# Kernel tuning notes

Hardware: AMD Instinct MI355X
Metric: run time of the kernel (lower is better)

## Reference

```python
import jax, jax.numpy as jnp
import numpy as np

N_NODES = 50000
N_EDGES = 800000
IN_F = 128
HID = 128
N_REL = 8


def setup_inputs() -> dict:
    key = jax.random.key(0)
    ks = jax.random.split(key, 12)
    s = 0.05
    return {
        "in_feat": jax.random.normal(ks[0], (N_NODES, IN_F), dtype=jnp.float32),
        "W1": jax.random.normal(ks[1], (N_REL, IN_F, HID), dtype=jnp.float32) * s,
        "W1_self": jax.random.normal(ks[2], (IN_F, HID), dtype=jnp.float32) * s,
        "b1": jnp.zeros((HID,), dtype=jnp.float32),
        "W2": jax.random.normal(ks[3], (N_REL, HID, HID), dtype=jnp.float32) * s,
        "W2_self": jax.random.normal(ks[4], (HID, HID), dtype=jnp.float32) * s,
        "b2": jnp.zeros((HID,), dtype=jnp.float32),
        "fc_w": jax.random.normal(ks[5], (HID, 1), dtype=jnp.float32) * s,
        "fc_b": jnp.zeros((1,), dtype=jnp.float32),
        "src": jax.random.randint(ks[6], (N_EDGES,), 0, N_NODES),
        "dst": jax.random.randint(ks[7], (N_EDGES,), 0, N_NODES),
        "etypes": jax.random.randint(ks[8], (N_EDGES,), 0, N_REL),
    }


def _rel_graph_conv(h, W, W_self, b, src, dst, etypes, n_nodes):
    # Transform node features once per relation: [R, N, H]
    xr = jnp.einsum('nd,rdh->rnh', h, W)
    # Per-edge message: gather relation-specific transformed source features [E, H]
    msgs = xr[etypes, src]
    # Scatter-sum aggregation to destination nodes [N, H]
    agg = jax.ops.segment_sum(msgs, dst, num_segments=n_nodes)
    # Self-loop + bias + ReLU (DGL RelGraphConv defaults)
    return jax.nn.relu(agg + h @ W_self + b)


def reference(in_feat, W1, W1_self, b1, W2, W2_self, b2, fc_w, fc_b, src, dst, etypes):
    n = in_feat.shape[0]
    h = _rel_graph_conv(in_feat, W1, W1_self, b1, src, dst, etypes, n)
    # dropout layers are identity in eval mode
    h = _rel_graph_conv(h, W2, W2_self, b2, src, dst, etypes, n)
    pooled = jnp.mean(h, axis=0, keepdims=True)  # AvgPooling over one graph -> [1, H]
    logits = pooled @ fc_w + fc_b                # [1, 1]
    return jax.nn.sigmoid(logits)
```

## Files before the change

### kernel.cpp

```cpp
#include <hip/hip_runtime.h>

#define NNODES 50000
#define NEDGES 800000
#define F 128
#define NREL 8
#define NOUT 1152
#define NBKT 98
#define BSH 9
#define SEG 16384
#define NTILES 391
#define GEMM_BLOCKS (8 * 9 * 49)
#define CSR_BLOCKS 196

typedef short bf16x8 __attribute__((ext_vector_type(8)));
typedef float f32x4 __attribute__((ext_vector_type(4)));
typedef float f32x2 __attribute__((ext_vector_type(2)));

__device__ __forceinline__ unsigned f2bf(float f) {
  unsigned u = __float_as_uint(f);
  u += 0x7fffu + ((u >> 16) & 1u);
  return u >> 16;
}
__device__ __forceinline__ float bf2f(unsigned v) {
  return __uint_as_float(v << 16);
}

typedef __attribute__((address_space(3))) void lds_void;
typedef const __attribute__((address_space(1))) void glb_void;
__device__ __forceinline__ void gll16(const void* g, void* l) {
  __builtin_amdgcn_global_load_lds(
      (glb_void*)(unsigned long long)g,
      (lds_void*)(unsigned)(unsigned long long)l, 16, 0, 0);
}

#define PREP_ZERO  33
#define PREP_CVT   12500
#define PREP_W     576
__global__ __launch_bounds__(256)
void k_prep(const float* __restrict__ in_feat, ushort* __restrict__ feat0,
            const float* __restrict__ W1, const float* __restrict__ W1s,
            ushort* __restrict__ Wt1,
            const float* __restrict__ W2, const float* __restrict__ W2s,
            ushort* __restrict__ Wt2,
            float* __restrict__ pooled_p, int* __restrict__ bcur) {
  const int b = blockIdx.x, t = threadIdx.x;
  if (b < 32) {
    pooled_p[b * 256 + t] = 0.f;
  } else if (b < PREP_ZERO) {
    if (t <= NBKT) bcur[t] = 0;
  } else if (b < PREP_ZERO + PREP_CVT) {
    int i = (b - PREP_ZERO) * 256 + t;
    float2 v = ((const float2*)in_feat)[i];
    ((unsigned*)feat0)[i] = f2bf(v.x) | (f2bf(v.y) << 16);
  } else {
    int w2 = (b >= PREP_ZERO + PREP_CVT + PREP_W);
    int idx = (b - PREP_ZERO - PREP_CVT - (w2 ? PREP_W : 0)) * 256 + t;
    int n = idx >> 7, k = idx & 127;
    int r = n >> 7, c = n & 127;
    const float* Wr = w2 ? W2 : W1;
    const float* Ws = w2 ? W2s : W1s;
    float v = (r < NREL) ? Wr[((size_t)r * F + k) * F + c] : Ws[(size_t)k * F + c];
    (w2 ? Wt2 : Wt1)[idx] = (ushort)f2bf(v);
  }
}

__global__ __launch_bounds__(256)
void k_fsort(const int* __restrict__ ebuf, const int* __restrict__ bcur,
             int* __restrict__ rowptr, int* __restrict__ edata) {
  __shared__ int cnt[512];
  __shared__ int pos[512];
  __shared__ int ws2[256];
  __shared__ int bc_s;
  const int b = blockIdx.x, t = threadIdx.x;
  int myc = (t < NBKT) ? bcur[t] : 0;
  ws2[t] = (t < b) ? myc : 0;
  if (t == b) bc_s = myc;
  __syncthreads();
  for (int off = 1; off < 256; off <<= 1) {
    int x = (t >= off) ? ws2[t - off] : 0;
    __syncthreads();
    ws2[t] += x;
    __syncthreads();
  }
  const int beg = ws2[255];
  const int cntb = bc_s;
  const int sbeg = b * SEG;

  cnt[t] = 0; cnt[t + 256] = 0;
  __syncthreads();
  for (int e = t; e < cntb; e += 256)
    atomicAdd(&cnt[((unsigned)ebuf[sbeg + e]) >> 19], 1);
  __syncthreads();
  int a = cnt[2 * t], b2 = cnt[2 * t + 1];
  ws2[t] = a + b2;
  __syncthreads();
  for (int off = 1; off < 256; off <<= 1) {
    int x = (t >= off) ? ws2[t - off] : 0;
    __syncthreads();
    ws2[t] += x;
    __syncthreads();
  }
  int ep = ws2[t] - (a + b2);
  pos[2 * t] = ep;
  pos[2 * t + 1] = ep + a;
  __syncthreads();
  int node0 = b << BSH;
#pragma unroll
  for (int i = t; i < 512; i += 256) {
    int node = node0 + i;
    if (node < NNODES) rowptr[node] = beg + pos[i];
  }
  if (b == NBKT - 1 && t == 0) rowptr[NNODES] = NEDGES;
  __syncthreads();
  for (int e = t; e < cntb; e += 256) {
    int rec = ebuf[sbeg + e];
    int c = ((unsigned)rec) >> 19;
    int lrank = atomicAdd(&pos[c], 1);
    int srcv = (rec >> 3) & 0xFFFF;
    int etv = rec & 7;
    edata[beg + lrank] = srcv * NOUT + etv * F;
  }
}

__global__ __launch_bounds__(512, 4)
void gemm_xrs(const ushort* __restrict__ A, const ushort* __restrict__ Wt,
              unsigned char* __restrict__ xrs, int doCsr,
              const int* __restrict__ src, const int* __restrict__ dst,
              const int* __restrict__ et, int* __restrict__ bcur,
              int* __restrict__ ebuf) {
  __shared__ uint4 As[2048];
  __shared__ uint4 Bs[2048];
  __shared__ int lhist[NBKT];
  __shared__ int lbase[NBKT];
  const int tid = threadIdx.x;

  if (doCsr && blockIdx.x < CSR_BLOCKS) {
    if (tid < NBKT) lhist[tid] = 0;
    __syncthreads();
    int e0 = blockIdx.x * 4096;
    int rec[8], cc[8], lr[8];
#pragma unroll
    for (int i = 0; i < 8; ++i) {
      int e = e0 + tid + i * 512;
      if (e < NEDGES) {
        int d = dst[e];
        cc[i] = d >> BSH;
        rec[i] = ((d & 511) << 19) | (src[e] << 3) | et[e];
        lr[i] = atomicAdd(&lhist[cc[i]], 1);
      } else {
        cc[i] = -1;
      }
    }
    __syncthreads();
    if (tid < NBKT && lhist[tid] > 0) lbase[tid] = atomicAdd(&bcur[tid], lhist[tid]);
    __syncthreads();
#pragma unroll
    for (int i = 0; i < 8; ++i)
      if (cc[i] >= 0) ebuf[cc[i] * SEG + lbase[cc[i]] + lr[i]] = rec[i];
    return;
  }

  const int id = blockIdx.x - (doCsr ? CSR_BLOCKS : 0);
  const int x = id & 7, j = id >> 3;
  const int tile = (j / 9) * 8 + x;
  const int cb = j % 9;
  if (tile >= NTILES) return;
  const int row0 = tile * 128;

  const int lane = tid & 63;
  const int w = tid >> 6;
  const int i16 = lane & 15, q = lane >> 4;
  const int mbase = (w & 3) * 32, nbase = (w >> 2) * 64;

#pragma unroll
  for (int i = 0; i < 4; ++i) {
    int L = tid + i * 512;
    int r = L >> 4, c4s = L & 15;
    int c4 = c4s ^ (r & 15);
    int agr = row0 + r; if (agr >= NNODES) agr = NNODES - 1;
    gll16((const void*)(A + (size_t)agr * F + c4 * 8), (void*)&As[L]);
    gll16((const void*)(Wt + ((size_t)cb * 128 + r) * F + c4 * 8), (void*)&Bs[L]);
  }
  __syncthreads();

  f32x4 acc[2][4];
#pragma unroll
  for (int a = 0; a < 2; ++a)
#pragma unroll
    for (int b = 0; b < 4; ++b) acc[a][b] = (f32x4)0.f;

#pragma unroll
  for (int c = 0; c < 4; ++c) {
    bf16x8 af[2], bfr[4];
#pragma unroll
    for (int mi = 0; mi < 2; ++mi) {
      int r = mbase + mi * 16 + i16;
      af[mi] = *(const bf16x8*)&As[r * 16 + ((c * 4 + q) ^ (r & 15))];
    }
#pragma unroll
    for (int ni = 0; ni < 4; ++ni) {
      int r = nbase + ni * 16 + i16;
      bfr[ni] = *(const bf16x8*)&Bs[r * 16 + ((c * 4 + q) ^ (r & 15))];
    }
#pragma unroll
    for (int mi = 0; mi < 2; ++mi)
#pragma unroll
      for (int ni = 0; ni < 4; ++ni)
        acc[mi][ni] = __builtin_amdgcn_mfma_f32_16x16x32_bf16(
            bfr[ni], af[mi], acc[mi][ni], 0, 0, 0);
  }

  unsigned pkv[2][4];
#pragma unroll
  for (int mi = 0; mi < 2; ++mi)
#pragma unroll
    for (int ni = 0; ni < 4; ++ni) {
      f32x4 v = acc[mi][ni];
      unsigned pk = 0;
      pk = __builtin_amdgcn_cvt_pk_fp8_f32(v[0], v[1], pk, false);
      pk = __builtin_amdgcn_cvt_pk_fp8_f32(v[2], v[3], pk, true);
      pkv[mi][ni] = pk;
    }

  __syncthreads();
  unsigned* sbuf = (unsigned*)As;
  {
    const int dbase = (nbase >> 2) + q;
#pragma unroll
    for (int mi = 0; mi < 2; ++mi) {
      int nl = mbase + mi * 16 + i16;
      int sw = (nl & 7) << 2;
      int vb_ = nl * 32;
#pragma unroll
      for (int ni = 0; ni < 4; ++ni)
        sbuf[vb_ + ((dbase + ni * 4) ^ sw)] = pkv[mi][ni];
    }
  }
  __syncthreads();

#pragma unroll
  for (int k = 0; k < 2; ++k) {
    int nl = k * 64 + (tid >> 3);
    int ch = tid & 7;
    int d0 = (ch * 4) ^ ((nl & 7) << 2);
    uint4 v = *(const uint4*)&sbuf[nl * 32 + d0];
    int row = row0 + nl;
    if (row < NNODES)
      *(uint4*)(xrs + (size_t)row * NOUT + cb * 128 + ch * 16) = v;
  }
}

__global__ __launch_bounds__(256)
void k_aggregate(const unsigned char* __restrict__ xrs,
                 const int* __restrict__ rowptr, const int* __restrict__ edata,
                 const float* __restrict__ bias, ushort* __restrict__ hout,
                 float* __restrict__ pooled_p) {
  __shared__ float red[4][128];
  const int wv = threadIdx.x >> 6;
  const int node = blockIdx.x * 4 + wv;
  const int lane = threadIdx.x & 63;
  const int half = lane >> 5, sl = lane & 31;
  const int beg = rowptr[node], end = rowptr[node + 1];

  float a0 = 0.f, a1 = 0.f, a2 = 0.f, a3 = 0.f;
  if (half == 0) {
    unsigned sv = *(const unsigned*)(xrs + (size_t)node * NOUT + NREL * F + sl * 4);
    f32x2 lo = __builtin_amdgcn_cvt_pk_f32_fp8(sv, false);
    f32x2 hi = __builtin_amdgcn_cvt_pk_f32_fp8(sv, true);
    a0 += lo[0]; a1 += lo[1]; a2 += hi[0]; a3 += hi[1];
  }

  for (int base = beg; base < end; base += 64) {
    int cnt = end - base; if (cnt > 64) cnt = 64;
    int my = (base + lane < end) ? edata[base + lane] : 0;
    int pairs = cnt >> 1;
    int p = 0;
    for (; p + 8 <= pairs; p += 8) {
      unsigned v[8];
#pragma unroll
      for (int k = 0; k < 8; ++k) {
        int off = __shfl(my, 2 * (p + k) + half, 64);
        v[k] = *(const unsigned*)(xrs + (size_t)off + sl * 4);
      }
#pragma unroll
      for (int k = 0; k < 8; ++k) {
        f32x2 lo = __builtin_amdgcn_cvt_pk_f32_fp8(v[k], false);
        f32x2 hi = __builtin_amdgcn_cvt_pk_f32_fp8(v[k], true);
        a0 += lo[0]; a1 += lo[1]; a2 += hi[0]; a3 += hi[1];
      }
    }
    for (; p < pairs; ++p) {
      int off = __shfl(my, 2 * p + half, 64);
      unsigned vv = *(const unsigned*)(xrs + (size_t)off + sl * 4);
      f32x2 lo = __builtin_amdgcn_cvt_pk_f32_fp8(vv, false);
      f32x2 hi = __builtin_amdgcn_cvt_pk_f32_fp8(vv, true);
      a0 += lo[0]; a1 += lo[1]; a2 += hi[0]; a3 += hi[1];
    }
    if (cnt & 1) {
      int off = __shfl(my, cnt - 1, 64);
      if (half == 0) {
        unsigned vv = *(const unsigned*)(xrs + (size_t)off + sl * 4);
        f32x2 lo = __builtin_amdgcn_cvt_pk_f32_fp8(vv, false);
        f32x2 hi = __builtin_amdgcn_cvt_pk_f32_fp8(vv, true);
        a0 += lo[0]; a1 += lo[1]; a2 += hi[0]; a3 += hi[1];
      }
    }
  }

  a0 += __shfl_xor(a0, 32, 64);
  a1 += __shfl_xor(a1, 32, 64);
  a2 += __shfl_xor(a2, 32, 64);
  a3 += __shfl_xor(a3, 32, 64);

  float4 bb = ((const float4*)bias)[sl];
  a0 = fmaxf(a0 + bb.x, 0.f);
  a1 = fmaxf(a1 + bb.y, 0.f);
  a2 = fmaxf(a2 + bb.z, 0.f);
  a3 = fmaxf(a3 + bb.w, 0.f);

  if (hout) {
    if (half == 0) {
      uint2 pk;
      pk.x = f2bf(a0) | (f2bf(a1) << 16);
      pk.y = f2bf(a2) | (f2bf(a3) << 16);
      ((uint2*)(hout + (size_t)node * F))[sl] = pk;
    }
  } else {
    if (half == 0) {
      red[wv][sl * 4 + 0] = a0;
      red[wv][sl * 4 + 1] = a1;
      red[wv][sl * 4 + 2] = a2;
      red[wv][sl * 4 + 3] = a3;
    }
    __syncthreads();
    if (threadIdx.x < 128) {
      float s = red[0][threadIdx.x] + red[1][threadIdx.x] +
                red[2][threadIdx.x] + red[3][threadIdx.x];
      atomicAdd(&pooled_p[(blockIdx.x & 63) * 128 + threadIdx.x], s);
    }
  }
}

__global__ __launch_bounds__(128)
void k_final(const float* __restrict__ pooled_p, const float* __restrict__ fcw,
             const float* __restrict__ fcb, float* __restrict__ out) {
  __shared__ float s[128];
  int t = threadIdx.x;
  float acc = 0.f;
#pragma unroll 8
  for (int k = 0; k < 64; ++k) acc += pooled_p[k * 128 + t];
  s[t] = acc * (1.0f / (float)NNODES) * fcw[t];
  __syncthreads();
  if (t == 0) {
    float v = 0.f;
    for (int i = 0; i < 128; ++i) v += s[i];
    v += fcb[0];
    out[0] = 1.f / (1.f + expf(-v));
  }
}

extern "C" void kernel_launch(void* const* d_in, const int* in_sizes, int n_in,
                              void* d_out, int out_size, void* d_ws, size_t ws_size,
                              hipStream_t stream) {
  const float* in_feat = (const float*)d_in[0];
  const float* W1      = (const float*)d_in[1];
  const float* W1s     = (const float*)d_in[2];
  const float* b1      = (const float*)d_in[3];
  const float* W2      = (const float*)d_in[4];
  const float* W2s     = (const float*)d_in[5];
  const float* b2      = (const float*)d_in[6];
  const float* fcw     = (const float*)d_in[7];
  const float* fcb     = (const float*)d_in[8];
  const int*   src     = (const int*)d_in[9];
  const int*   dst     = (const int*)d_in[10];
  const int*   et      = (const int*)d_in[11];
  float* out = (float*)d_out;

  unsigned char* xrs = (unsigned char*)d_ws;
  ushort* feat0 = (ushort*)(xrs + (size_t)NNODES * NOUT);
  ushort* h1    = feat0 + (size_t)NNODES * F;
  ushort* Wt1   = h1 + (size_t)NNODES * F;
  ushort* Wt2   = Wt1 + (size_t)NOUT * F;
  float* pooled_p = (float*)(Wt2 + (size_t)NOUT * F);
  int*   bcur   = (int*)(pooled_p + 64 * 128);
  int*   rowptr = bcur + NBKT + 1;
  int*   ebuf   = rowptr + NNODES + 2;
  int*   edata  = ebuf + NBKT * SEG;

  k_prep<<<PREP_ZERO + PREP_CVT + 2 * PREP_W, 256, 0, stream>>>(
      in_feat, feat0, W1, W1s, Wt1, W2, W2s, Wt2, pooled_p, bcur);

  const int aggBlocks = NNODES / 4;

  gemm_xrs<<<CSR_BLOCKS + GEMM_BLOCKS, 512, 0, stream>>>(
      feat0, Wt1, xrs, 1, src, dst, et, bcur, ebuf);
  k_fsort<<<NBKT, 256, 0, stream>>>(ebuf, bcur, rowptr, edata);
  k_aggregate<<<aggBlocks, 256, 0, stream>>>(xrs, rowptr, edata, b1, h1, nullptr);
  gemm_xrs<<<GEMM_BLOCKS, 512, 0, stream>>>(
      h1, Wt2, xrs, 0, src, dst, et, bcur, ebuf);
  k_aggregate<<<aggBlocks, 256, 0, stream>>>(xrs, rowptr, edata, b2, nullptr, pooled_p);

  k_final<<<1, 128, 0, stream>>>(pooled_p, fcw, fcb, out);
}
```

Baseline: 231.8 us.

## Switch GEMM operands and intermediate features from bf16 to fp8

Input features, weights and the layer-1 hidden output are now stored as fp8 (e4m3) instead of bf16, and the GEMM uses the fp8 MFMA with halved LDS tiles and an adjusted swizzle. This halves the bytes of the A/B operands loaded per tile and shrinks the prep conversion and h1 write traffic, and the halved LDS allows a higher occupancy launch bound. It costs accuracy, since inputs and weights are quantized to 8-bit floats before the matmul, which may push the result past tolerance.

```diff
diff --git a/kernel.cpp b/kernel.cpp
--- a/kernel.cpp
+++ b/kernel.cpp
@@ -12,7 +12,6 @@
 #define GEMM_BLOCKS (8 * 9 * 49)
 #define CSR_BLOCKS 196
 
-typedef short bf16x8 __attribute__((ext_vector_type(8)));
 typedef float f32x4 __attribute__((ext_vector_type(4)));
 typedef float f32x2 __attribute__((ext_vector_type(2)));
 
@@ -20,9 +19,6 @@
   unsigned u = __float_as_uint(f);
   u += 0x7fffu + ((u >> 16) & 1u);
   return u >> 16;
-}
-__device__ __forceinline__ float bf2f(unsigned v) {
-  return __uint_as_float(v << 16);
 }
 
 typedef __attribute__((address_space(3))) void lds_void;
@@ -34,14 +30,14 @@
 }
 
 #define PREP_ZERO  33
-#define PREP_CVT   12500
-#define PREP_W     576
+#define PREP_CVT   6250
+#define PREP_W     144
 __global__ __launch_bounds__(256)
-void k_prep(const float* __restrict__ in_feat, ushort* __restrict__ feat0,
+void k_prep(const float* __restrict__ in_feat, unsigned* __restrict__ feat0,
             const float* __restrict__ W1, const float* __restrict__ W1s,
-            ushort* __restrict__ Wt1,
+            unsigned* __restrict__ Wt1,
             const float* __restrict__ W2, const float* __restrict__ W2s,
-            ushort* __restrict__ Wt2,
+            unsigned* __restrict__ Wt2,
             float* __restrict__ pooled_p, int* __restrict__ bcur) {
   const int b = blockIdx.x, t = threadIdx.x;
   if (b < 32) {
@@ -50,17 +46,34 @@
     if (t <= NBKT) bcur[t] = 0;
   } else if (b < PREP_ZERO + PREP_CVT) {
     int i = (b - PREP_ZERO) * 256 + t;
-    float2 v = ((const float2*)in_feat)[i];
-    ((unsigned*)feat0)[i] = f2bf(v.x) | (f2bf(v.y) << 16);
+    float4 v = ((const float4*)in_feat)[i];
+    unsigned pk = 0;
+    pk = __builtin_amdgcn_cvt_pk_fp8_f32(v.x, v.y, pk, false);
+    pk = __builtin_amdgcn_cvt_pk_fp8_f32(v.z, v.w, pk, true);
+    feat0[i] = pk;
   } else {
     int w2 = (b >= PREP_ZERO + PREP_CVT + PREP_W);
     int idx = (b - PREP_ZERO - PREP_CVT - (w2 ? PREP_W : 0)) * 256 + t;
-    int n = idx >> 7, k = idx & 127;
+    int n = idx >> 5, k0 = (idx & 31) * 4;
     int r = n >> 7, c = n & 127;
     const float* Wr = w2 ? W2 : W1;
     const float* Ws = w2 ? W2s : W1s;
-    float v = (r < NREL) ? Wr[((size_t)r * F + k) * F + c] : Ws[(size_t)k * F + c];
-    (w2 ? Wt2 : Wt1)[idx] = (ushort)f2bf(v);
+    float v0, v1, v2, v3;
+    if (r < NREL) {
+      v0 = Wr[((size_t)(r * F + k0 + 0)) * F + c];
+      v1 = Wr[((size_t)(r * F + k0 + 1)) * F + c];
+      v2 = Wr[((size_t)(r * F + k0 + 2)) * F + c];
+      v3 = Wr[((size_t)(r * F + k0 + 3)) * F + c];
+    } else {
+      v0 = Ws[(size_t)(k0 + 0) * F + c];
+      v1 = Ws[(size_t)(k0 + 1) * F + c];
+      v2 = Ws[(size_t)(k0 + 2) * F + c];
+      v3 = Ws[(size_t)(k0 + 3) * F + c];
+    }
+    unsigned pk = 0;
+    pk = __builtin_amdgcn_cvt_pk_fp8_f32(v0, v1, pk, false);
+    pk = __builtin_amdgcn_cvt_pk_fp8_f32(v2, v3, pk, true);
+    (w2 ? Wt2 : Wt1)[idx] = pk;
   }
 }
 
@@ -122,14 +135,15 @@
   }
 }
 
-__global__ __launch_bounds__(512, 4)
-void gemm_xrs(const ushort* __restrict__ A, const ushort* __restrict__ Wt,
+__global__ __launch_bounds__(512, 8)
+void gemm_xrs(const unsigned char* __restrict__ A,
+              const unsigned char* __restrict__ Wt,
               unsigned char* __restrict__ xrs, int doCsr,
               const int* __restrict__ src, const int* __restrict__ dst,
               const int* __restrict__ et, int* __restrict__ bcur,
               int* __restrict__ ebuf) {
-  __shared__ uint4 As[2048];
-  __shared__ uint4 Bs[2048];
+  __shared__ uint4 As[1024];
+  __shared__ uint4 Bs[1024];
   __shared__ int lhist[NBKT];
   __shared__ int lbase[NBKT];
   const int tid = threadIdx.x;
@@ -173,13 +187,13 @@
   const int mbase = (w & 3) * 32, nbase = (w >> 2) * 64;
 
 #pragma unroll
-  for (int i = 0; i < 4; ++i) {
+  for (int i = 0; i < 2; ++i) {
     int L = tid + i * 512;
-    int r = L >> 4, c4s = L & 15;
-    int c4 = c4s ^ (r & 15);
+    int r = L >> 3, c8s = L & 7;
+    int c8 = c8s ^ (r & 7);
     int agr = row0 + r; if (agr >= NNODES) agr = NNODES - 1;
-    gll16((const void*)(A + (size_t)agr * F + c4 * 8), (void*)&As[L]);
-    gll16((const void*)(Wt + ((size_t)cb * 128 + r) * F + c4 * 8), (void*)&Bs[L]);
+    gll16((const void*)(A + (size_t)agr * F + c8 * 16), (void*)&As[L]);
+    gll16((const void*)(Wt + ((size_t)cb * 128 + r) * F + c8 * 16), (void*)&Bs[L]);
   }
   __syncthreads();
 
@@ -189,24 +203,28 @@
 #pragma unroll
     for (int b = 0; b < 4; ++b) acc[a][b] = (f32x4)0.f;
 
+  const char* Ab = (const char*)As;
+  const char* Bb = (const char*)Bs;
 #pragma unroll
   for (int c = 0; c < 4; ++c) {
-    bf16x8 af[2], bfr[4];
+    const int ch = c * 2 + (q >> 1);
+    const int h8 = (q & 1) << 3;
+    long af[2], bfr[4];
 #pragma unroll
     for (int mi = 0; mi < 2; ++mi) {
       int r = mbase + mi * 16 + i16;
-      af[mi] = *(const bf16x8*)&As[r * 16 + ((c * 4 + q) ^ (r & 15))];
+      af[mi] = *(const long*)(Ab + r * 128 + ((ch ^ (r & 7)) << 4) + h8);
     }
 #pragma unroll
     for (int ni = 0; ni < 4; ++ni) {
       int r = nbase + ni * 16 + i16;
-      bfr[ni] = *(const bf16x8*)&Bs[r * 16 + ((c * 4 + q) ^ (r & 15))];
+      bfr[ni] = *(const long*)(Bb + r * 128 + ((ch ^ (r & 7)) << 4) + h8);
     }
 #pragma unroll
     for (int mi = 0; mi < 2; ++mi)
 #pragma unroll
       for (int ni = 0; ni < 4; ++ni)
-        acc[mi][ni] = __builtin_amdgcn_mfma_f32_16x16x32_bf16(
+        acc[mi][ni] = __builtin_amdgcn_mfma_f32_16x16x32_fp8_fp8(
             bfr[ni], af[mi], acc[mi][ni], 0, 0, 0);
   }
 
@@ -253,7 +271,7 @@
 __global__ __launch_bounds__(256)
 void k_aggregate(const unsigned char* __restrict__ xrs,
                  const int* __restrict__ rowptr, const int* __restrict__ edata,
-                 const float* __restrict__ bias, ushort* __restrict__ hout,
+                 const float* __restrict__ bias, unsigned char* __restrict__ hout,
                  float* __restrict__ pooled_p) {
   __shared__ float red[4][128];
   const int wv = threadIdx.x >> 6;
@@ -320,10 +338,10 @@
 
   if (hout) {
     if (half == 0) {
-      uint2 pk;
-      pk.x = f2bf(a0) | (f2bf(a1) << 16);
-      pk.y = f2bf(a2) | (f2bf(a3) << 16);
-      ((uint2*)(hout + (size_t)node * F))[sl] = pk;
+      unsigned pk = 0;
+      pk = __builtin_amdgcn_cvt_pk_fp8_f32(a0, a1, pk, false);
+      pk = __builtin_amdgcn_cvt_pk_fp8_f32(a2, a3, pk, true);
+      ((unsigned*)(hout + (size_t)node * F))[sl] = pk;
     }
   } else {
     if (half == 0) {
@@ -377,10 +395,10 @@
   float* out = (float*)d_out;
 
   unsigned char* xrs = (unsigned char*)d_ws;
-  ushort* feat0 = (ushort*)(xrs + (size_t)NNODES * NOUT);
-  ushort* h1    = feat0 + (size_t)NNODES * F;
-  ushort* Wt1   = h1 + (size_t)NNODES * F;
-  ushort* Wt2   = Wt1 + (size_t)NOUT * F;
+  unsigned char* feat0 = xrs + (size_t)NNODES * NOUT;
+  unsigned char* h1  = feat0 + (size_t)NNODES * F;
+  unsigned char* Wt1 = h1 + (size_t)NNODES * F;
+  unsigned char* Wt2 = Wt1 + (size_t)NOUT * F;
   float* pooled_p = (float*)(Wt2 + (size_t)NOUT * F);
   int*   bcur   = (int*)(pooled_p + 64 * 128);
   int*   rowptr = bcur + NBKT + 1;
@@ -388,7 +406,8 @@
   int*   edata  = ebuf + NBKT * SEG;
 
   k_prep<<<PREP_ZERO + PREP_CVT + 2 * PREP_W, 256, 0, stream>>>(
-      in_feat, feat0, W1, W1s, Wt1, W2, W2s, Wt2, pooled_p, bcur);
+      in_feat, (unsigned*)feat0, W1, W1s, (unsigned*)Wt1,
+      W2, W2s, (unsigned*)Wt2, pooled_p, bcur);
 
   const int aggBlocks = NNODES / 4;
 
```

New measurement: 220.1 us. 1.05x faster.
